# Kernel optimization log

Measured on AMD Instinct MI355X. Metric: run time of the kernel, lower is better.

## Reference

```python
import jax, jax.numpy as jnp
import numpy as np

DIM = 1536
N_HEADS = 12
HEAD_DIM = DIM // N_HEADS          # 128
C = HEAD_DIM // 2                  # 64 complex channels
C_F = C - 2 * (C // 3)             # 22
C_H = C // 3                       # 21
C_W = C // 3                       # 21
EPS = 1e-6
MAX_F, MAX_HW = 64, 64


def _rope_table(max_len, c_sub):
    # Wan rope_params: theta_j = 10000^{-j/c_sub}, angle = pos * theta
    inv = 1.0 / (10000.0 ** (np.arange(c_sub, dtype=np.float32) / c_sub))
    ang = np.arange(max_len, dtype=np.float32)[:, None] * inv[None, :]
    return jnp.asarray(np.cos(ang)), jnp.asarray(np.sin(ang))


def setup_inputs() -> dict:
    key = jax.random.key(0)
    ks = jax.random.split(key, 12)
    s = 1.0 / np.sqrt(DIM)
    F_, H_, W_ = 9, 16, 28
    S = F_ * H_ * W_
    x = jax.random.normal(ks[0], (1, S, DIM), dtype=jnp.float32)
    Wq = jax.random.normal(ks[1], (DIM, DIM), dtype=jnp.float32) * s
    Wk = jax.random.normal(ks[2], (DIM, DIM), dtype=jnp.float32) * s
    Wv = jax.random.normal(ks[3], (DIM, DIM), dtype=jnp.float32) * s
    Wo = jax.random.normal(ks[4], (DIM, DIM), dtype=jnp.float32) * s
    bq = jnp.zeros((DIM,), jnp.float32)
    bk = jnp.zeros((DIM,), jnp.float32)
    bv = jnp.zeros((DIM,), jnp.float32)
    bo = jnp.zeros((DIM,), jnp.float32)
    gq = jnp.ones((DIM,), jnp.float32)
    gk = jnp.ones((DIM,), jnp.float32)
    cos_f, sin_f = _rope_table(MAX_F, C_F)
    cos_h, sin_h = _rope_table(MAX_HW, C_H)
    cos_w, sin_w = _rope_table(MAX_HW, C_W)
    return dict(x=x, Wq=Wq, bq=bq, Wk=Wk, bk=bk, Wv=Wv, bv=bv, Wo=Wo, bo=bo,
                gq=gq, gk=gk, cos_f=cos_f, sin_f=sin_f, cos_h=cos_h,
                sin_h=sin_h, cos_w=cos_w, sin_w=sin_w, F=F_, H=H_, W=W_)


def _rms(t, g):
    t = t.astype(jnp.float32)
    return t * jax.lax.rsqrt(jnp.mean(t * t, axis=-1, keepdims=True) + EPS) * g


def _grid_cos_sin(cos_f, sin_f, cos_h, sin_h, cos_w, sin_w, F, H, W):
    # concat per-axis angle tables expanded over the (F,H,W) grid -> [S, C]
    def expand(tab, shape):
        return jnp.broadcast_to(tab.reshape(shape + (tab.shape[-1],)), (F, H, W, tab.shape[-1]))
    cos = jnp.concatenate([expand(cos_f[:F], (F, 1, 1)),
                           expand(cos_h[:H], (1, H, 1)),
                           expand(cos_w[:W], (1, 1, W))], axis=-1).reshape(F * H * W, C)
    sin = jnp.concatenate([expand(sin_f[:F], (F, 1, 1)),
                           expand(sin_h[:H], (1, H, 1)),
                           expand(sin_w[:W], (1, 1, W))], axis=-1).reshape(F * H * W, C)
    return cos, sin


def _rope(t, cos, sin):
    # t: [B,S,N,D]; adjacent pairs (even=real, odd=imag) rotated by complex freqs
    b, s, n, d = t.shape
    tr = t.reshape(b, s, n, C, 2)
    e, o = tr[..., 0], tr[..., 1]
    co = cos[None, :, None, :]
    si = sin[None, :, None, :]
    return jnp.stack([e * co - o * si, e * si + o * co], axis=-1).reshape(b, s, n, d)


def reference(x, Wq, bq, Wk, bk, Wv, bv, Wo, bo, gq, gk,
              cos_f, sin_f, cos_h, sin_h, cos_w, sin_w, F, H, W):
    b, s, dim = x.shape
    q = _rms(x @ Wq.T + bq, gq).reshape(b, s, N_HEADS, HEAD_DIM)
    k = _rms(x @ Wk.T + bk, gk).reshape(b, s, N_HEADS, HEAD_DIM)
    v = (x @ Wv.T + bv).reshape(b, s, N_HEADS, HEAD_DIM)
    cos, sin = _grid_cos_sin(cos_f, sin_f, cos_h, sin_h, cos_w, sin_w, F, H, W)
    rq = _rope(q, cos, sin)
    rk = _rope(k, cos, sin)
    scale = 1.0 / jnp.sqrt(jnp.asarray(HEAD_DIM, jnp.float32))
    scores = jnp.einsum('bqhd,bkhd->bhqk', rq, rk) * scale
    att = jax.nn.softmax(scores, axis=-1)
    out = jnp.einsum('bhqk,bkhd->bqhd', att, v).reshape(b, s, dim)
    return out @ Wo.T + bo
```

## Files before the change

kernel.cpp:

```cpp
#include <hip/hip_runtime.h>
#include <math.h>

using u16 = unsigned short;
using u32 = unsigned int;

typedef __attribute__((ext_vector_type(8))) short short8;
typedef __attribute__((ext_vector_type(4))) float float4v;

#define S_LEN 4032
#define DIM   1536
#define NH    12
#define HD    128
#define F_DIM 9
#define H_DIM 16
#define W_DIM 28
#define NX4 1548288
#define NW4 589824

__device__ __forceinline__ float b2f(u16 v) {
  return __uint_as_float(((u32)v) << 16);
}
__device__ __forceinline__ u16 f2bf(float f) {
  u32 u = __float_as_uint(f);
  u32 r = (u + 0x7FFFu + ((u >> 16) & 1u)) >> 16;
  return (u16)r;
}
__device__ __forceinline__ u32 pack2(float lo, float hi) {
  return __builtin_amdgcn_perm(__float_as_uint(hi), __float_as_uint(lo),
                               0x07060302u);
}

__device__ __forceinline__ void gld16(const void* g, void* l) {
  __builtin_amdgcn_global_load_lds(
      (const __attribute__((address_space(1))) void*)g,
      (__attribute__((address_space(3))) void*)l, 16, 0, 0);
}

__device__ __forceinline__ void plswap(u32 a, u32 b, u32& x, u32& y, int lane) {
#if __has_builtin(__builtin_amdgcn_permlane32_swap) && __has_builtin(__builtin_amdgcn_permlane16_swap)
  auto t = __builtin_amdgcn_permlane32_swap(a, b, false, false);
  auto u = __builtin_amdgcn_permlane16_swap(t[0], t[1], false, false);
  x = u[0]; y = u[1];
#else
  u32 ax = (u32)__shfl_xor((int)a, 32, 64), bx = (u32)__shfl_xor((int)b, 32, 64);
  u32 t0 = (lane & 32) ? bx : a;
  u32 t1 = (lane & 32) ? b : ax;
  u32 t0x = (u32)__shfl_xor((int)t0, 16, 64), t1x = (u32)__shfl_xor((int)t1, 16, 64);
  x = (lane & 16) ? t1x : t0;
  y = (lane & 16) ? t1 : t0x;
#endif
}

__global__ void __launch_bounds__(256) cast_all(
    const float* __restrict__ x, const float* __restrict__ wq,
    const float* __restrict__ wk, const float* __restrict__ wv,
    const float* __restrict__ wo,
    u16* __restrict__ xb, u16* __restrict__ wqb,
    u16* __restrict__ wkb, u16* __restrict__ wvb,
    u16* __restrict__ wob)
{
  int i = blockIdx.x * 256 + threadIdx.x;
  const float* s; u16* d; int j;
  if (i < NX4)              { s = x;  d = xb;  j = i; }
  else if (i < NX4 + NW4)   { s = wq; d = wqb; j = i - NX4; }
  else if (i < NX4 + 2*NW4) { s = wk; d = wkb; j = i - NX4 - NW4; }
  else if (i < NX4 + 3*NW4) { s = wv; d = wvb; j = i - NX4 - 2*NW4; }
  else                      { s = wo; d = wob; j = i - NX4 - 3*NW4; }
  const float4 v = ((const float4*)s)[j];
  ushort4 o;
  o.x = f2bf(v.x); o.y = f2bf(v.y); o.z = f2bf(v.z); o.w = f2bf(v.w);
  ((ushort4*)d)[j] = o;
}

template <bool F32OUT>
__device__ __forceinline__ void gemm_core(
    const u16* __restrict__ A, const u16* __restrict__ Bw,
    const float* __restrict__ bias, void* __restrict__ OutV,
    int bm, int bn)
{
  __shared__ u16 As[2][128 * 64];
  __shared__ u16 Bs[2][128 * 64];
  const int tid  = threadIdx.x;
  const int wave = tid >> 6, lane = tid & 63;
  const int quad = lane >> 4, l15 = lane & 15;
  const int wm = wave >> 1, wn = wave & 1;

  float4v acc[4][4] = {};

  const int arow = lane >> 3;
  const int acol = ((lane & 7) ^ arow) * 8;

  auto stage = [&](int b, int kt) {
#pragma unroll
    for (int c = 0; c < 4; ++c) {
      int seg = wave * 4 + c;
      int row = seg * 8 + arow;
      int ga = bm + row; if (ga > S_LEN - 1) ga = S_LEN - 1;
      gld16(&A[(size_t)ga * DIM + kt + acol], &As[b][seg * 512]);
      gld16(&Bw[(size_t)(bn + row) * DIM + kt + acol], &Bs[b][seg * 512]);
    }
  };

  stage(0, 0);
  __syncthreads();

  int cur = 0;
  for (int kt = 0; kt < DIM; kt += 64) {
    if (kt + 64 < DIM) stage(cur ^ 1, kt + 64);

#pragma unroll
    for (int ks = 0; ks < 64; ks += 32) {
      const int kc = ks >> 3;
      short8 af[4], bf[4];
#pragma unroll
      for (int mt = 0; mt < 4; ++mt) {
        const int ra = wm * 64 + mt * 16 + l15;
        af[mt] = *(const short8*)((const char*)As[cur] + ra * 128 + (((kc + quad) ^ (ra & 7)) << 4));
      }
#pragma unroll
      for (int nt = 0; nt < 4; ++nt) {
        const int rb = wn * 64 + nt * 16 + l15;
        bf[nt] = *(const short8*)((const char*)Bs[cur] + rb * 128 + (((kc + quad) ^ (rb & 7)) << 4));
      }
#pragma unroll
      for (int mt = 0; mt < 4; ++mt)
#pragma unroll
        for (int nt = 0; nt < 4; ++nt)
          acc[mt][nt] = __builtin_amdgcn_mfma_f32_16x16x32_bf16(af[mt], bf[nt], acc[mt][nt], 0, 0, 0);
    }

    __syncthreads();
    cur ^= 1;
  }

#pragma unroll
  for (int mt = 0; mt < 4; ++mt) {
    const int row = bm + wm * 64 + mt * 16 + quad * 4;
#pragma unroll
    for (int nt = 0; nt < 4; ++nt) {
      const int col = bn + wn * 64 + nt * 16 + l15;
      const float bv = bias[col];
#pragma unroll
      for (int r = 0; r < 4; ++r) {
        float v = acc[mt][nt][r] + bv;
        if (row + r < S_LEN) {
          if (F32OUT) ((float*)OutV)[(size_t)(row + r) * DIM + col] = v;
          else        ((u16*)OutV)[(size_t)(row + r) * DIM + col] = f2bf(v);
        }
      }
    }
  }
}

__global__ void __launch_bounds__(256) gemm_qkv(
    const u16* __restrict__ X,
    const u16* __restrict__ Wq, const u16* __restrict__ Wk, const u16* __restrict__ Wv,
    const float* __restrict__ bq, const float* __restrict__ bk, const float* __restrict__ bv,
    u16* __restrict__ Qb, u16* __restrict__ Kb, u16* __restrict__ Vb)
{
  const int z = blockIdx.z;
  const u16* B    = (z == 0) ? Wq : (z == 1) ? Wk : Wv;
  const float* bi = (z == 0) ? bq : (z == 1) ? bk : bv;
  u16* O          = (z == 0) ? Qb : (z == 1) ? Kb : Vb;
  gemm_core<false>(X, B, bi, O, blockIdx.y * 128, blockIdx.x * 128);
}

__global__ void __launch_bounds__(256) gemm_wo(
    const u16* __restrict__ A, const u16* __restrict__ Wo,
    const float* __restrict__ bo, float* __restrict__ Out)
{
  gemm_core<true>(A, Wo, bo, Out, blockIdx.y * 128, blockIdx.x * 128);
}

__global__ void __launch_bounds__(256) rms_rope(
    u16* Q, u16* K,
    const float* __restrict__ gq, const float* __restrict__ gk,
    const float* __restrict__ cf, const float* __restrict__ sf,
    const float* __restrict__ ch, const float* __restrict__ sh,
    const float* __restrict__ cw, const float* __restrict__ sw)
{
  __shared__ float red[2][4];
  const int s = blockIdx.x;
  const int t = threadIdx.x;
  const int wave = t >> 6, lane = t & 63;
  const size_t rowb = (size_t)s * DIM + t * 6;

  u32* q32 = (u32*)(Q + rowb);
  u32* k32 = (u32*)(K + rowb);
  u32 qw[3], kw[3];
#pragma unroll
  for (int j = 0; j < 3; ++j) { qw[j] = q32[j]; kw[j] = k32[j]; }

  float sq = 0.f, sk = 0.f;
#pragma unroll
  for (int j = 0; j < 3; ++j) {
    float a0 = b2f((u16)qw[j]), a1 = b2f((u16)(qw[j] >> 16));
    float b0 = b2f((u16)kw[j]), b1 = b2f((u16)(kw[j] >> 16));
    sq += a0 * a0 + a1 * a1;
    sk += b0 * b0 + b1 * b1;
  }
#pragma unroll
  for (int m = 1; m < 64; m <<= 1) {
    sq += __shfl_xor(sq, m, 64);
    sk += __shfl_xor(sk, m, 64);
  }
  if (lane == 0) { red[0][wave] = sq; red[1][wave] = sk; }
  __syncthreads();
  const float tq = red[0][0] + red[0][1] + red[0][2] + red[0][3];
  const float tk = red[1][0] + red[1][1] + red[1][2] + red[1][3];
  const float scq = rsqrtf(tq * (1.0f / DIM) + 1e-6f);
  const float sck = rsqrtf(tk * (1.0f / DIM) + 1e-6f);

  const int f  = s / (H_DIM * W_DIM);
  const int hh = (s / W_DIM) % H_DIM;
  const int w  = s % W_DIM;

#pragma unroll
  for (int j = 0; j < 3; ++j) {
    const int pi = t * 3 + j;
    const int c = pi & 63;
    float co, si;
    if (c < 22)      { co = cf[f * 22 + c];        si = sf[f * 22 + c]; }
    else if (c < 43) { co = ch[hh * 21 + c - 22];  si = sh[hh * 21 + c - 22]; }
    else             { co = cw[w * 21 + c - 43];   si = sw[w * 21 + c - 43]; }
    const int gi = 2 * pi;
    const float2 gqv = *(const float2*)&gq[gi];
    const float2 gkv = *(const float2*)&gk[gi];
    {
      float e = b2f((u16)qw[j])         * scq * gqv.x;
      float o = b2f((u16)(qw[j] >> 16)) * scq * gqv.y;
      q32[j] = (u32)f2bf(e * co - o * si) | ((u32)f2bf(e * si + o * co) << 16);
    }
    {
      float e = b2f((u16)kw[j])         * sck * gkv.x;
      float o = b2f((u16)(kw[j] >> 16)) * sck * gkv.y;
      k32[j] = (u32)f2bf(e * co - o * si) | ((u32)f2bf(e * si + o * co) << 16);
    }
  }
}

__global__ void __launch_bounds__(256) transpose_v(
    const u16* __restrict__ V, u16* __restrict__ Vt)
{
  __shared__ u16 tile[64][65];
  const int s0 = blockIdx.x * 64, d0 = blockIdx.y * 64;
  const int t = threadIdx.x;
#pragma unroll
  for (int i = 0; i < 16; ++i) {
    int idx = t + i * 256; int rr = idx >> 6, cc = idx & 63;
    tile[rr][cc] = V[(size_t)(s0 + rr) * DIM + d0 + cc];
  }
  __syncthreads();
#pragma unroll
  for (int i = 0; i < 16; ++i) {
    int idx = t + i * 256; int rr = idx >> 6, cc = idx & 63;
    Vt[(size_t)(d0 + rr) * S_LEN + s0 + cc] = tile[cc][rr];
  }
}

__global__ void __launch_bounds__(256, 2) attn_kernel(
    const u16* __restrict__ rq, const u16* __restrict__ rk,
    const u16* __restrict__ vt,
    u16* __restrict__ po, float* __restrict__ pl, int klen)
{
  __shared__ u16 Ks[64 * 128];
  __shared__ u16 Vs[128 * 64];

  const int id    = blockIdx.x;
  const int xcd   = id & 7;
  const int rest  = id >> 3;
  const int band  = rest / 21;
  const int slot  = rest - band * 21;
  const int slice = band * 8 + xcd;
  const int h     = slice % NH;
  const int split = slice / NH;
  const int k_begin = split * klen;
  const int k_end   = (k_begin + klen < S_LEN) ? (k_begin + klen) : S_LEN;
  const int qb = slot * 192;
  const int tid = threadIdx.x, wave = tid >> 6, lane = tid & 63;
  const int quad = lane >> 4, l15 = lane & 15;
  const int q0 = qb + wave * 48;

  const int kr_l   = (lane >> 4);
  const int kc_l   = lane & 15;
  const int vdr_l  = (lane >> 3);
  const int vc_l   = lane & 7;

  short8 qf[3][4];
#pragma unroll
  for (int mt = 0; mt < 3; ++mt) {
    int row = q0 + mt * 16 + l15; if (row > S_LEN - 1) row = S_LEN - 1;
#pragma unroll
    for (int c = 0; c < 4; ++c)
      qf[mt][c] = *(const short8*)&rq[(size_t)row * DIM + h * HD + c * 32 + quad * 8];
  }

  float4v o[3][8] = {};
  float l_[3] = {0.f, 0.f, 0.f};

  const float SC = 0.08838834764831845f * 1.4426950408889634f;
  const float M0 = 20.0f;

#pragma unroll
  for (int c = 0; c < 4; ++c) {
    const int seg = wave * 4 + c;
    const int kr = seg * 4 + kr_l;
    gld16(&rk[(size_t)(k_begin + kr) * DIM + h * HD + ((kc_l ^ (kr & 15)) << 3)],
          &Ks[seg * 512]);
  }
  __syncthreads();

  for (int kt = k_begin; kt < k_end; kt += 64) {
#pragma unroll
    for (int c = 0; c < 4; ++c) {
      const int seg = wave * 4 + c;
      const int vd = seg * 8 + vdr_l;
      gld16(&vt[(size_t)(h * HD + vd) * S_LEN + kt + ((vc_l ^ (vd & 7)) << 3)],
            &Vs[seg * 512]);
    }

    short8 pf[3][2];

#pragma unroll
    for (int half = 0; half < 2; ++half) {
      float4v sc[3][2] = {};
      __builtin_amdgcn_s_setprio(1);
#pragma unroll
      for (int nth = 0; nth < 2; ++nth) {
        const int krow = (half * 2 + nth) * 16 + l15;
#pragma unroll
        for (int c = 0; c < 4; ++c) {
          const short8 kf = *(const short8*)((char*)Ks + krow * 256 + (((c * 4 + quad) ^ l15) << 4));
#pragma unroll
          for (int mt = 0; mt < 3; ++mt)
            sc[mt][nth] = __builtin_amdgcn_mfma_f32_16x16x32_bf16(kf, qf[mt][c], sc[mt][nth], 0, 0, 0);
        }
      }
      __builtin_amdgcn_s_setprio(0);

#pragma unroll
      for (int mt = 0; mt < 3; ++mt) {
        u32 W[2][2];
#pragma unroll
        for (int nth = 0; nth < 2; ++nth) {
          const float p0 = __builtin_amdgcn_exp2f(fmaf(sc[mt][nth][0], SC, -M0));
          const float p1 = __builtin_amdgcn_exp2f(fmaf(sc[mt][nth][1], SC, -M0));
          const float p2 = __builtin_amdgcn_exp2f(fmaf(sc[mt][nth][2], SC, -M0));
          const float p3 = __builtin_amdgcn_exp2f(fmaf(sc[mt][nth][3], SC, -M0));
          l_[mt] += (p0 + p1) + (p2 + p3);
          W[nth][0] = pack2(p0, p1);
          W[nth][1] = pack2(p2, p3);
        }
        u32 w0, w1, w2, w3;
        plswap(W[0][0], W[1][0], w0, w2, lane);
        plswap(W[0][1], W[1][1], w1, w3, lane);
        union { u32 w[4]; short8 s; } cv;
        cv.w[0] = w0; cv.w[1] = w1; cv.w[2] = w2; cv.w[3] = w3;
        pf[mt][half] = cv.s;
      }
    }

    __syncthreads();

    if (kt + 64 < k_end) {
#pragma unroll
      for (int c = 0; c < 4; ++c) {
        const int seg = wave * 4 + c;
        const int kr = seg * 4 + kr_l;
        gld16(&rk[(size_t)(kt + 64 + kr) * DIM + h * HD + ((kc_l ^ (kr & 15)) << 3)],
              &Ks[seg * 512]);
      }
    }

    __builtin_amdgcn_s_setprio(1);
#pragma unroll
    for (int dt = 0; dt < 8; ++dt) {
      const int drow = dt * 16 + l15;
#pragma unroll
      for (int ko = 0; ko < 2; ++ko) {
        const short8 vf = *(const short8*)((char*)Vs + drow * 128 + (((ko * 4 + quad) ^ (l15 & 7)) << 4));
#pragma unroll
        for (int mt = 0; mt < 3; ++mt)
          o[mt][dt] = __builtin_amdgcn_mfma_f32_16x16x32_bf16(vf, pf[mt][ko], o[mt][dt], 0, 0, 0);
      }
    }
    __builtin_amdgcn_s_setprio(0);

    __syncthreads();
  }

#pragma unroll
  for (int mt = 0; mt < 3; ++mt) {
    float t = l_[mt];
    t += __shfl_xor(t, 16, 64);
    t += __shfl_xor(t, 32, 64);
    l_[mt] = t;
  }
#pragma unroll
  for (int mt = 0; mt < 3; ++mt) {
    const int q = q0 + mt * 16 + l15;
    const bool valid = q < S_LEN;
    const size_t rbase = ((size_t)(split * NH + h) * S_LEN + q) * HD;
#pragma unroll
    for (int dt = 0; dt < 8; ++dt) {
      if (valid) {
        ushort4 pk;
        pk.x = f2bf(o[mt][dt][0]); pk.y = f2bf(o[mt][dt][1]);
        pk.z = f2bf(o[mt][dt][2]); pk.w = f2bf(o[mt][dt][3]);
        *(ushort4*)&po[rbase + dt * 16 + quad * 4] = pk;
      }
    }
    if (quad == 0 && valid)
      pl[(size_t)(split * NH + h) * S_LEN + q] = l_[mt];
  }
}

__global__ void __launch_bounds__(256) attn_merge(
    const u16* __restrict__ po, const float* __restrict__ pl,
    u16* __restrict__ ao, int nsplit)
{
  const int gw = (blockIdx.x * 256 + threadIdx.x) >> 6;
  const int lane = threadIdx.x & 63;
  const int h = gw / S_LEN;
  const int q = gw - h * S_LEN;
  float den = 0.f, a0 = 0.f, a1 = 0.f;
  for (int s = 0; s < nsplit; ++s) {
    const size_t r = (size_t)(s * NH + h) * S_LEN + q;
    den += pl[r];
    const ushort2 v = *(const ushort2*)&po[r * HD + lane * 2];
    a0 += b2f(v.x); a1 += b2f(v.y);
  }
  const float inv = (den > 0.f) ? (1.0f / den) : 0.f;
  ushort2 out;
  out.x = f2bf(a0 * inv);
  out.y = f2bf(a1 * inv);
  *(ushort2*)&ao[(size_t)q * DIM + h * HD + lane * 2] = out;
}

extern "C" void kernel_launch(void* const* d_in, const int* in_sizes, int n_in,
                              void* d_out, int out_size, void* d_ws, size_t ws_size,
                              hipStream_t stream) {
  const float* x  = (const float*)d_in[0];
  const float* Wq = (const float*)d_in[1];
  const float* bq = (const float*)d_in[2];
  const float* Wk = (const float*)d_in[3];
  const float* bk = (const float*)d_in[4];
  const float* Wv = (const float*)d_in[5];
  const float* bv = (const float*)d_in[6];
  const float* Wo = (const float*)d_in[7];
  const float* bo = (const float*)d_in[8];
  const float* gq = (const float*)d_in[9];
  const float* gk = (const float*)d_in[10];
  const float* cf = (const float*)d_in[11];
  const float* sf = (const float*)d_in[12];
  const float* ch = (const float*)d_in[13];
  const float* sh = (const float*)d_in[14];
  const float* cw = (const float*)d_in[15];
  const float* sw = (const float*)d_in[16];

  char* ws = (char*)d_ws;
  const size_t sz  = (size_t)S_LEN * DIM * 2;
  const size_t wsz = (size_t)DIM * DIM * 2;
  u16* Xb  = (u16*)(ws);
  u16* Qb  = (u16*)(ws + sz);
  u16* Kb  = (u16*)(ws + 2 * sz);
  u16* Vb  = (u16*)(ws + 3 * sz);
  u16* Wqb = (u16*)(ws + 4 * sz);
  u16* Wkb = (u16*)(ws + 4 * sz + wsz);
  u16* Wvb = (u16*)(ws + 4 * sz + 2 * wsz);

  const int nsplit = 2;
  const int klen   = 2048;
  const size_t po_one = (size_t)NH * S_LEN * HD * 2;
  const size_t pl_one = (size_t)NH * S_LEN * 4;
  char* pbase = ws + 4 * sz;
  u16*   po = (u16*)pbase;
  float* pl = (float*)(pbase + (size_t)nsplit * po_one);
  u16* Wob = (u16*)(ws + 4 * sz + (size_t)nsplit * (po_one + pl_one));
  u16* Vt  = Xb;
  u16* Ao  = Qb;

  cast_all<<<(NX4 + 4 * NW4) / 256, 256, 0, stream>>>(
      x, Wq, Wk, Wv, Wo, Xb, Wqb, Wkb, Wvb, Wob);

  gemm_qkv<<<dim3(12, 32, 3), 256, 0, stream>>>(Xb, Wqb, Wkb, Wvb, bq, bk, bv, Qb, Kb, Vb);

  rms_rope<<<S_LEN, 256, 0, stream>>>(Qb, Kb, gq, gk, cf, sf, ch, sh, cw, sw);
  transpose_v<<<dim3(63, 24), 256, 0, stream>>>(Vb, Vt);
  attn_kernel<<<504, 256, 0, stream>>>(Qb, Kb, Vt, po, pl, klen);
  attn_merge<<<(NH * S_LEN) / 4, 256, 0, stream>>>(po, pl, Ao, nsplit);
  gemm_wo<<<dim3(12, 32), 256, 0, stream>>>(Ao, Wob, bo, (float*)d_out);
}
```

Baseline: 394.7 us.

## Fuse Q/K/V projections into one GEMM sharing the X tile

Replaces the z-indexed QKV GEMM launch, which ran three separate 128x128 tile GEMMs, with a single kernel in which each block loads one 128x64 X tile and multiplies it against 64-column slices of Wq, Wk and Wv. The aim is to cut repeated global and LDS loads of X by reusing each X tile across all three weight matrices. The grid changes from 12x32x3 to 24x32 blocks. Each thread now holds 24 accumulators, and the larger shared buffers may reduce occupancy.

```diff
diff --git a/kernel.cpp b/kernel.cpp
--- a/kernel.cpp
+++ b/kernel.cpp
@@ -72,6 +72,103 @@
   ((ushort4*)d)[j] = o;
 }
 
+__global__ void __launch_bounds__(256) gemm_qkv_fused(
+    const u16* __restrict__ X,
+    const u16* __restrict__ Wq, const u16* __restrict__ Wk, const u16* __restrict__ Wv,
+    const float* __restrict__ bq, const float* __restrict__ bk, const float* __restrict__ bv,
+    u16* __restrict__ Qb, u16* __restrict__ Kb, u16* __restrict__ Vb)
+{
+  __shared__ u16 As[2][128 * 64];
+  __shared__ u16 Bs[2][3][64 * 64];
+  const int tid  = threadIdx.x;
+  const int wave = tid >> 6, lane = tid & 63;
+  const int quad = lane >> 4, l15 = lane & 15;
+  const int wm = wave >> 1, wn = wave & 1;
+  const int bm = blockIdx.y * 128, bn = blockIdx.x * 64;
+
+  float4v acc[3][4][2] = {};
+
+  const int arow = lane >> 3;
+  const int acol = ((lane & 7) ^ arow) * 8;
+
+  auto stage = [&](int b, int kt) {
+#pragma unroll
+    for (int c = 0; c < 4; ++c) {
+      int seg = wave * 4 + c;
+      int row = seg * 8 + arow;
+      int ga = bm + row; if (ga > S_LEN - 1) ga = S_LEN - 1;
+      gld16(&X[(size_t)ga * DIM + kt + acol], &As[b][seg * 512]);
+    }
+#pragma unroll
+    for (int z = 0; z < 3; ++z) {
+      const u16* W = (z == 0) ? Wq : (z == 1) ? Wk : Wv;
+#pragma unroll
+      for (int c = 0; c < 2; ++c) {
+        int seg = wave * 2 + c;
+        int row = seg * 8 + arow;
+        gld16(&W[(size_t)(bn + row) * DIM + kt + acol], &Bs[b][z][seg * 512]);
+      }
+    }
+  };
+
+  stage(0, 0);
+  __syncthreads();
+
+  int cur = 0;
+  for (int kt = 0; kt < DIM; kt += 64) {
+    if (kt + 64 < DIM) stage(cur ^ 1, kt + 64);
+
+#pragma unroll
+    for (int ks = 0; ks < 64; ks += 32) {
+      const int kc = ks >> 3;
+      short8 af[4];
+#pragma unroll
+      for (int mt = 0; mt < 4; ++mt) {
+        const int ra = wm * 64 + mt * 16 + l15;
+        af[mt] = *(const short8*)((const char*)As[cur] + ra * 128 + (((kc + quad) ^ (ra & 7)) << 4));
+      }
+#pragma unroll
+      for (int z = 0; z < 3; ++z) {
+        short8 bf[2];
+#pragma unroll
+        for (int nt = 0; nt < 2; ++nt) {
+          const int rb = wn * 32 + nt * 16 + l15;
+          bf[nt] = *(const short8*)((const char*)Bs[cur][z] + rb * 128 + (((kc + quad) ^ (rb & 7)) << 4));
+        }
+#pragma unroll
+        for (int mt = 0; mt < 4; ++mt)
+#pragma unroll
+          for (int nt = 0; nt < 2; ++nt)
+            acc[z][mt][nt] = __builtin_amdgcn_mfma_f32_16x16x32_bf16(af[mt], bf[nt], acc[z][mt][nt], 0, 0, 0);
+      }
+    }
+
+    __syncthreads();
+    cur ^= 1;
+  }
+
+#pragma unroll
+  for (int z = 0; z < 3; ++z) {
+    u16* O          = (z == 0) ? Qb : (z == 1) ? Kb : Vb;
+    const float* bi = (z == 0) ? bq : (z == 1) ? bk : bv;
+#pragma unroll
+    for (int mt = 0; mt < 4; ++mt) {
+      const int row = bm + wm * 64 + mt * 16 + quad * 4;
+#pragma unroll
+      for (int nt = 0; nt < 2; ++nt) {
+        const int col = bn + wn * 32 + nt * 16 + l15;
+        const float bv_ = bi[col];
+#pragma unroll
+        for (int r = 0; r < 4; ++r) {
+          float v = acc[z][mt][nt][r] + bv_;
+          if (row + r < S_LEN)
+            O[(size_t)(row + r) * DIM + col] = f2bf(v);
+        }
+      }
+    }
+  }
+}
+
 template <bool F32OUT>
 __device__ __forceinline__ void gemm_core(
     const u16* __restrict__ A, const u16* __restrict__ Bw,
@@ -150,19 +247,6 @@
       }
     }
   }
-}
-
-__global__ void __launch_bounds__(256) gemm_qkv(
-    const u16* __restrict__ X,
-    const u16* __restrict__ Wq, const u16* __restrict__ Wk, const u16* __restrict__ Wv,
-    const float* __restrict__ bq, const float* __restrict__ bk, const float* __restrict__ bv,
-    u16* __restrict__ Qb, u16* __restrict__ Kb, u16* __restrict__ Vb)
-{
-  const int z = blockIdx.z;
-  const u16* B    = (z == 0) ? Wq : (z == 1) ? Wk : Wv;
-  const float* bi = (z == 0) ? bq : (z == 1) ? bk : bv;
-  u16* O          = (z == 0) ? Qb : (z == 1) ? Kb : Vb;
-  gemm_core<false>(X, B, bi, O, blockIdx.y * 128, blockIdx.x * 128);
 }
 
 __global__ void __launch_bounds__(256) gemm_wo(
@@ -483,7 +567,8 @@
   cast_all<<<(NX4 + 4 * NW4) / 256, 256, 0, stream>>>(
       x, Wq, Wk, Wv, Wo, Xb, Wqb, Wkb, Wvb, Wob);
 
-  gemm_qkv<<<dim3(12, 32, 3), 256, 0, stream>>>(Xb, Wqb, Wkb, Wvb, bq, bk, bv, Qb, Kb, Vb);
+  gemm_qkv_fused<<<dim3(24, 32), 256, 0, stream>>>(
+      Xb, Wqb, Wkb, Wvb, bq, bk, bv, Qb, Kb, Vb);
 
   rms_rope<<<S_LEN, 256, 0, stream>>>(Qb, Kb, gq, gk, cf, sf, ch, sh, cw, sw);
   transpose_v<<<dim3(63, 24), 256, 0, stream>>>(Vb, Vt);
```

New measurement: 382.4 us. -3.1%, faster.
